# Optimization experiments

Measured on AMD Instinct MI355X. Metric: run time of the kernel, lower is better.

## Reference

```python
import jax, jax.numpy as jnp
import numpy as np
import math

L, D, H = 4, 256, 8
HD = D // H
B, SQ, SK = 2, 1024, 1024
FF = 3 * D
EPS = 1e-5


def setup_inputs() -> dict:
    key = jax.random.key(0)
    ks = jax.random.split(key, 16)
    s = 0.02
    w = lambda k, shape: jax.random.normal(k, shape, jnp.float32) * s
    return {
        "pose": jax.random.normal(ks[0], (B, SQ, D), jnp.float32),
        "vel": jax.random.normal(ks[1], (B, SK, D), jnp.float32),
        "img": jax.random.normal(ks[2], (B, SK, D), jnp.float32),
        "Wq": w(ks[3], (L, D, D)), "bq": jnp.zeros((L, D), jnp.float32),
        "Wk": w(ks[4], (L, D, D)), "bk": jnp.zeros((L, D), jnp.float32),
        "Wv": w(ks[5], (L, D, D)), "bv": jnp.zeros((L, D), jnp.float32),
        "Wo": w(ks[6], (L, D, D)), "bo": jnp.zeros((L, D), jnp.float32),
        "an_g": jnp.ones((L, D), jnp.float32), "an_b": jnp.zeros((L, D), jnp.float32),
        "W1": w(ks[7], (L, D, FF)), "b1": jnp.zeros((L, FF), jnp.float32),
        "W2": w(ks[8], (L, FF, D)), "b2": jnp.zeros((L, D), jnp.float32),
        "fn_g": jnp.ones((L, D), jnp.float32), "fn_b": jnp.zeros((L, D), jnp.float32),
        "n_g": jnp.ones((L, D), jnp.float32), "n_b": jnp.zeros((L, D), jnp.float32),
    }


def entmax15(x):
    # exact alpha=1.5 entmax along the last axis (Peters & Martins 2019)
    x = x * 0.5
    x = x - jnp.max(x, axis=-1, keepdims=True)
    z = -jnp.sort(-x, axis=-1)  # descending
    k = jnp.arange(1, z.shape[-1] + 1, dtype=x.dtype)
    mean = jnp.cumsum(z, axis=-1) / k
    mean_sq = jnp.cumsum(z * z, axis=-1) / k
    ss = k * (mean_sq - mean * mean)
    delta = jnp.clip((1.0 - ss) / k, 0.0)
    tau = mean - jnp.sqrt(delta)
    support = jnp.sum(tau <= z, axis=-1, keepdims=True)  # support size >= 1
    tau_star = jnp.take_along_axis(tau, support - 1, axis=-1)
    p = jnp.clip(x - tau_star, 0.0)
    return p * p


def layer_norm(x, g, b):
    m = jnp.mean(x, axis=-1, keepdims=True)
    v = jnp.mean((x - m) ** 2, axis=-1, keepdims=True)
    return (x - m) * jax.lax.rsqrt(v + EPS) * g + b


def mish(x):
    return x * jnp.tanh(jax.nn.softplus(x))


def reference(pose, vel, img, Wq, bq, Wk, bk, Wv, bv, Wo, bo, an_g, an_b,
              W1, b1, W2, b2, fn_g, fn_b, n_g, n_b):
    def mha(q_in, kv, i):
        bs, sq, _ = q_in.shape
        sk = kv.shape[1]
        q = (q_in @ Wq[i] + bq[i]).reshape(bs, sq, H, HD)
        k = (kv @ Wk[i] + bk[i]).reshape(bs, sk, H, HD)
        v = (kv @ Wv[i] + bv[i]).reshape(bs, sk, H, HD)
        scores = jnp.einsum('bqhd,bkhd->bhqk', q, k) / math.sqrt(HD)
        attn = entmax15(scores)
        out = jnp.einsum('bhqk,bkhd->bqhd', attn, v).reshape(bs, sq, D)
        return out @ Wo[i] + bo[i]

    def cross_layer(x1, x2, i):
        y = layer_norm(mha(x1, x2, i), an_g[i], an_b[i])
        x1 = x1 + y
        y = layer_norm(x1, fn_g[i], fn_b[i])
        h = mish(y @ W1[i] + b1[i]) @ W2[i] + b2[i]
        return x1 + h

    def stack(x, kv):
        for i in range(L):  # small fixed layer loop (shared weights across both paths)
            mem = x
            x = cross_layer(x, kv, i)
            x = layer_norm(x, n_g[i], n_b[i])
            x = x + mem
        return x

    img_out = stack(pose, img)
    pose_out = stack(pose, vel)
    return (pose_out, img_out)
```

## Files before the change

kernel.cpp:

```cpp
#include <hip/hip_runtime.h>
#include <math.h>

#define NL   4
#define DIM  256
#define NH   8
#define HDIM 32
#define SQL  1024
#define SKL  1024
#define FFD  768
#define CB   4
#define ROWS (CB * SQL)

typedef __attribute__((ext_vector_type(8))) short bf16x8;
typedef __attribute__((ext_vector_type(4))) short bf16x4;
typedef __attribute__((ext_vector_type(4))) float f32x4;
typedef __attribute__((ext_vector_type(2))) float f32x2;


__device__ __forceinline__ short f2bf(float f) {
    union { float f; unsigned u; } v; v.f = f;
    unsigned u = v.u + 0x7fffu + ((v.u >> 16) & 1u);
    return (short)(u >> 16);
}

__device__ __forceinline__ float fast_mish(float x) {
    float u = __expf(fminf(x, 20.0f));
    float a = __builtin_fmaf(u, u, 2.0f * u);
    return x * a * __builtin_amdgcn_rcpf(a + 2.0f);
}

__device__ __forceinline__ f32x2 lo2(f32x4 v) { return __builtin_shufflevector(v, v, 0, 1); }
__device__ __forceinline__ f32x2 hi2(f32x4 v) { return __builtin_shufflevector(v, v, 2, 3); }


__global__ __launch_bounds__(256) void init_kernel(
        const float* __restrict__ pose, const float* __restrict__ vel,
        const float* __restrict__ img, float* __restrict__ X,
        short* __restrict__ Xb, short* __restrict__ KVb) {
    int idx = blockIdx.x * 256 + threadIdx.x;
    if (idx >= CB * SQL * DIM) return;
    int c = idx / (SQL * DIM);
    int rem = idx - c * (SQL * DIM);
    int b = c & 1;
    float pv = pose[b * SQL * DIM + rem];
    X[idx]  = pv;
    Xb[idx] = f2bf(pv);
    const float* kv = (c < 2) ? vel : img;
    KVb[idx] = f2bf(kv[b * SQL * DIM + rem]);
}


__global__ __launch_bounds__(256) void transpose_all(
        const float* __restrict__ Wq, const float* __restrict__ Wk,
        const float* __restrict__ Wv, const float* __restrict__ Wo,
        const float* __restrict__ W1, const float* __restrict__ W2,
        short* __restrict__ Wqt, short* __restrict__ Wkt,
        short* __restrict__ Wvt, short* __restrict__ Wot,
        short* __restrict__ W1t, short* __restrict__ W2t) {
    __shared__ float tile[64][65];
    int z = blockIdx.x;
    const float* src; short* dst; int K, N, tx, ty;
    if (z < 256) {
        int m = z >> 6, lyr = (z >> 4) & 3, r = z & 15;
        src = ((m == 0) ? Wq : (m == 1) ? Wk : (m == 2) ? Wv : Wo) + (size_t)lyr * DIM * DIM;
        dst = ((m == 0) ? Wqt : (m == 1) ? Wkt : (m == 2) ? Wvt : Wot) + (size_t)lyr * DIM * DIM;
        K = DIM; N = DIM; tx = r & 3; ty = r >> 2;
    } else if (z < 448) {
        int idx = z - 256, lyr = idx / 48, r = idx % 48;
        src = W1 + (size_t)lyr * DIM * FFD; dst = W1t + (size_t)lyr * DIM * FFD;
        K = DIM; N = FFD; tx = r % 12; ty = r / 12;
    } else {
        int idx = z - 448, lyr = idx / 48, r = idx % 48;
        src = W2 + (size_t)lyr * FFD * DIM; dst = W2t + (size_t)lyr * FFD * DIM;
        K = FFD; N = DIM; tx = r % 4; ty = r / 4;
    }
    int t = threadIdx.x;
    int n0 = tx * 64, k0 = ty * 64;
#pragma unroll
    for (int i = 0; i < 16; i++) {
        int idx = t + i * 256;
        int r = idx >> 6, c = idx & 63;
        tile[r][c] = src[(size_t)(k0 + r) * N + n0 + c];
    }
    __syncthreads();
#pragma unroll
    for (int i = 0; i < 16; i++) {
        int idx = t + i * 256;
        int r = idx >> 6, c = idx & 63;
        dst[(size_t)(n0 + r) * K + k0 + c] = f2bf(tile[c][r]);
    }
}


__global__ __launch_bounds__(256) void qkv_gemm(
        const short* __restrict__ Xb, const short* __restrict__ KVb,
        const short* __restrict__ Wqt, const short* __restrict__ Wkt,
        const short* __restrict__ Wvt,
        const float* __restrict__ bq, const float* __restrict__ bk,
        const float* __restrict__ bv,
        short* __restrict__ Qb, short* __restrict__ Kb, short* __restrict__ Vt,
        float qscale) {
    int z = blockIdx.z;
    const short* A    = (z == 0) ? Xb : KVb;
    const short* Wt   = (z == 0) ? Wqt : (z == 1) ? Wkt : Wvt;
    const float* bias = (z == 0) ? bq : (z == 1) ? bk : bv;
    float scale = (z == 0) ? qscale : 1.0f;

    int t = threadIdx.x, l = t & 63, w = t >> 6;
    int lq = l & 15, lg = l >> 4;
    int bm = blockIdx.y * 64, bn = blockIdx.x * 64;

    const short* ap = A + (size_t)(bm + w * 16 + lq) * DIM + lg * 8;
    const short* wp = Wt + (size_t)(bn + lq) * DIM + lg * 8;

    f32x4 acc[4];
#pragma unroll
    for (int nt = 0; nt < 4; nt++) acc[nt] = (f32x4){0.f, 0.f, 0.f, 0.f};
#pragma unroll
    for (int k0 = 0; k0 < DIM; k0 += 32) {
        bf16x8 af = *(const bf16x8*)(ap + k0);
#pragma unroll
        for (int nt = 0; nt < 4; nt++) {
            bf16x8 bfr = *(const bf16x8*)(wp + (size_t)nt * 16 * DIM + k0);
            acc[nt] = __builtin_amdgcn_mfma_f32_16x16x32_bf16(af, bfr, acc[nt], 0, 0, 0);
        }
    }

    int ms = bm + w * 16 + lg * 4;
#pragma unroll
    for (int nt = 0; nt < 4; nt++) {
        int col = bn + nt * 16 + lq;
        float bv_ = bias[col];
        float v[4];
#pragma unroll
        for (int j = 0; j < 4; j++) v[j] = acc[nt][j] + bv_;
        if (z < 2) {
            short* out = (z == 0) ? Qb : Kb;
#pragma unroll
            for (int j = 0; j < 4; j++) out[(size_t)(ms + j) * DIM + col] = f2bf(v[j] * scale);
        } else {
            int cc = ms >> 10, kl = ms & 1023;
            bf16x4 pk;
#pragma unroll
            for (int j = 0; j < 4; j++) pk[j] = f2bf(v[j]);
            *(bf16x4*)(Vt + ((size_t)(cc * DIM + col)) * SKL + kl) = pk;
        }
    }
}


__global__ __launch_bounds__(512) void fused_tail(
        const short* __restrict__ T1b, const short* __restrict__ Wot,
        const float* __restrict__ bo, const float* __restrict__ Xres,
        const float* __restrict__ ag, const float* __restrict__ ab,
        const float* __restrict__ fg, const float* __restrict__ fb,
        const short* __restrict__ W1t, const float* __restrict__ b1,
        const short* __restrict__ W2t, const float* __restrict__ b2,
        const float* __restrict__ g_, const float* __restrict__ b_,
        float* __restrict__ outf, short* __restrict__ outb) {
    __shared__ float gbuf[16][264];
    __shared__ __align__(16) short y_lds[16][280];
    __shared__ __align__(16) short g1[16][792];
    float (*xbuf)[264] = (float(*)[264])g1;

    int t = threadIdx.x, l = t & 63, w = t >> 6;
    int lq = l & 15, lg = l >> 4;
    int bm = blockIdx.x * 16;

    {
        const short* ap = T1b + (size_t)(bm + lq) * DIM + lg * 8;
        const short* wp = Wot + (size_t)(w * 32 + lq) * DIM + lg * 8;
        f32x4 acc[2];
        acc[0] = (f32x4){0.f, 0.f, 0.f, 0.f};
        acc[1] = (f32x4){0.f, 0.f, 0.f, 0.f};
#pragma unroll
        for (int k0 = 0; k0 < DIM; k0 += 32) {
            bf16x8 af = *(const bf16x8*)(ap + k0);
#pragma unroll
            for (int nt = 0; nt < 2; nt++) {
                bf16x8 bfr = *(const bf16x8*)(wp + (size_t)nt * 16 * DIM + k0);
                acc[nt] = __builtin_amdgcn_mfma_f32_16x16x32_bf16(af, bfr, acc[nt], 0, 0, 0);
            }
        }
#pragma unroll
        for (int nt = 0; nt < 2; nt++) {
            int col = w * 32 + nt * 16 + lq;
            float bv_ = bo[col];
#pragma unroll
            for (int j = 0; j < 4; j++) gbuf[lg * 4 + j][col] = acc[nt][j] + bv_;
        }
    }
    __syncthreads();

    {
        int g = t >> 5, u = t & 31;
        int row = bm + g;
        float s = 0.f, s2 = 0.f;
#pragma unroll
        for (int i = 0; i < 8; i++) {
            float v = gbuf[g][u + 32 * i];
            s += v; s2 += v * v;
        }
#pragma unroll
        for (int off = 1; off < 32; off <<= 1) { s += __shfl_xor(s, off); s2 += __shfl_xor(s2, off); }
        float m = s * (1.f / DIM);
        float rstd = rsqrtf(s2 * (1.f / DIM) - m * m + 1e-5f);

        float x1v[8];
        float sb = 0.f, sb2 = 0.f;
#pragma unroll
        for (int i = 0; i < 8; i++) {
            int col = u + 32 * i;
            float x1 = Xres[(size_t)row * DIM + col] + (gbuf[g][col] - m) * rstd * ag[col] + ab[col];
            x1v[i] = x1; sb += x1; sb2 += x1 * x1;
        }
#pragma unroll
        for (int off = 1; off < 32; off <<= 1) { sb += __shfl_xor(sb, off); sb2 += __shfl_xor(sb2, off); }
        float m2 = sb * (1.f / DIM);
        float rstd2 = rsqrtf(sb2 * (1.f / DIM) - m2 * m2 + 1e-5f);
#pragma unroll
        for (int i = 0; i < 8; i++) {
            int col = u + 32 * i;
            gbuf[g][col]  = x1v[i];
            y_lds[g][col] = f2bf((x1v[i] - m2) * rstd2 * fg[col] + fb[col]);
        }
    }
    __syncthreads();

    {
        const short* wp = W1t + (size_t)(w * 96 + lq) * DIM + lg * 8;
        f32x4 acc[6];
#pragma unroll
        for (int nt = 0; nt < 6; nt++) acc[nt] = (f32x4){0.f, 0.f, 0.f, 0.f};
#pragma unroll
        for (int k0 = 0; k0 < DIM; k0 += 32) {
            bf16x8 af = *(const bf16x8*)(&y_lds[lq][k0 + lg * 8]);
#pragma unroll
            for (int nt = 0; nt < 6; nt++) {
                bf16x8 bfr = *(const bf16x8*)(wp + (size_t)nt * 16 * DIM + k0);
                acc[nt] = __builtin_amdgcn_mfma_f32_16x16x32_bf16(af, bfr, acc[nt], 0, 0, 0);
            }
        }
#pragma unroll
        for (int nt = 0; nt < 6; nt++) {
            int col = w * 96 + nt * 16 + lq;
            float bv_ = b1[col];
#pragma unroll
            for (int j = 0; j < 4; j++)
                g1[lg * 4 + j][col] = f2bf(fast_mish(acc[nt][j] + bv_));
        }
    }
    __syncthreads();

    f32x4 acc2[2];
    acc2[0] = (f32x4){0.f, 0.f, 0.f, 0.f};
    acc2[1] = (f32x4){0.f, 0.f, 0.f, 0.f};
    {
        const short* wp2 = W2t + (size_t)(w * 32 + lq) * FFD + lg * 8;
#pragma unroll 6
        for (int ks = 0; ks < 24; ks++) {
            bf16x8 af = *(const bf16x8*)(&g1[lq][ks * 32 + lg * 8]);
#pragma unroll
            for (int nt = 0; nt < 2; nt++) {
                bf16x8 bfr = *(const bf16x8*)(wp2 + (size_t)nt * 16 * FFD + ks * 32);
                acc2[nt] = __builtin_amdgcn_mfma_f32_16x16x32_bf16(af, bfr, acc2[nt], 0, 0, 0);
            }
        }
    }
    __syncthreads();
#pragma unroll
    for (int nt = 0; nt < 2; nt++) {
        int col = w * 32 + nt * 16 + lq;
        float bv_ = b2[col];
#pragma unroll
        for (int j = 0; j < 4; j++)
            xbuf[lg * 4 + j][col] = acc2[nt][j] + bv_ + gbuf[lg * 4 + j][col];
    }
    __syncthreads();

    {
        int g = t >> 5, u = t & 31;
        int row = bm + g;
        float s = 0.f, s2 = 0.f;
#pragma unroll
        for (int i = 0; i < 8; i++) {
            float v = xbuf[g][u + 32 * i];
            s += v; s2 += v * v;
        }
#pragma unroll
        for (int off = 1; off < 32; off <<= 1) { s += __shfl_xor(s, off); s2 += __shfl_xor(s2, off); }
        float m = s * (1.f / DIM);
        float rstd = rsqrtf(s2 * (1.f / DIM) - m * m + 1e-5f);
#pragma unroll
        for (int i = 0; i < 8; i++) {
            int col = u + 32 * i;
            float o = Xres[(size_t)row * DIM + col] + (xbuf[g][col] - m) * rstd * g_[col] + b_[col];
            outf[(size_t)row * DIM + col] = o;
            if (outb) outb[(size_t)row * DIM + col] = f2bf(o);
        }
    }
}


__global__ __launch_bounds__(512, 6) void attn_mfma(
        const short* __restrict__ Q, const short* __restrict__ K,
        const short* __restrict__ Vt, short* __restrict__ O) {
    int id = blockIdx.x;
    int xcd = id & 7, rest = id >> 3;
    int hc = xcd * 4 + (rest >> 6);
    int c = hc & 3, h = hc >> 2;
    int qbase = (rest & 63) * 16;
    int t = threadIdx.x, l = t & 63, w = t >> 6;
    int lq = l & 15, lg = l >> 4;

    __shared__ __align__(16) short p_lds[8][1024];
    __shared__ float obuf[8][512];
    __shared__ __align__(16) float sred[2][3][16][8];

    bf16x8 qfrag = *(const bf16x8*)(Q + ((size_t)(c * SQL + qbase + lq)) * DIM + h * HDIM + lg * 8);

    const int kw = w * 128;
    f32x4 acc[8];
#pragma unroll
    for (int kt = 0; kt < 8; kt++) {
        bf16x8 kf = *(const bf16x8*)(K + ((size_t)(c * SKL + kw + kt * 16 + lq)) * DIM + h * HDIM + lg * 8);
        f32x4 z = {0.f, 0.f, 0.f, 0.f};
        acc[kt] = __builtin_amdgcn_mfma_f32_16x16x32_bf16(kf, qfrag, z, 0, 0, 0);
    }

    const f32x2 z2  = {0.f, 0.f};
    const f32x2 big = {1e30f, 1e30f};
    const f32x2 one = {1.f, 1.f};

    f32x2 mm = lo2(acc[0]);
#pragma unroll
    for (int kt = 0; kt < 8; kt++) {
        mm = __builtin_elementwise_max(mm, lo2(acc[kt]));
        mm = __builtin_elementwise_max(mm, hi2(acc[kt]));
    }
    float m = fmaxf(mm.x, mm.y);
    m = fmaxf(m, __shfl_xor(m, 16));
    m = fmaxf(m, __shfl_xor(m, 32));
    if (l < 16) sred[1][0][l][w] = m;
    __syncthreads();
    {
        f32x4 a = *(const f32x4*)sred[1][0][lq];
        f32x4 b = *(const f32x4*)(sred[1][0][lq] + 4);
        f32x4 mx = __builtin_elementwise_max(a, b);
        m = fmaxf(fmaxf(mx[0], mx[1]), fmaxf(mx[2], mx[3]));
    }

    float tau = m - 1.0f;
    int r = 0;
    for (;;) {
        f32x2 vt = {tau, tau};
        f32x2 S1 = z2, S2 = z2, NN = z2;
#pragma unroll
        for (int kt = 0; kt < 8; kt++) {
            f32x2 y0 = __builtin_elementwise_max(lo2(acc[kt]) - vt, z2);
            f32x2 y1 = __builtin_elementwise_max(hi2(acc[kt]) - vt, z2);
            S1 += y0; S1 += y1;
            S2 += y0 * y0; S2 += y1 * y1;
            NN += __builtin_elementwise_min(y0 * big, one);
            NN += __builtin_elementwise_min(y1 * big, one);
        }
        float sy = S1.x + S1.y, sy2 = S2.x + S2.y, nn = NN.x + NN.y;
        sy  += __shfl_xor(sy, 16);  sy  += __shfl_xor(sy, 32);
        sy2 += __shfl_xor(sy2, 16); sy2 += __shfl_xor(sy2, 32);
        nn  += __shfl_xor(nn, 16);  nn  += __shfl_xor(nn, 32);
        int b = r & 1;
        if (l < 16) { sred[b][0][l][w] = nn; sred[b][1][l][w] = sy; sred[b][2][l][w] = sy2; }
        __syncthreads();
        {
            f32x4 n0 = *(const f32x4*)sred[b][0][lq];
            f32x4 n1 = *(const f32x4*)(sred[b][0][lq] + 4);
            f32x4 s0 = *(const f32x4*)sred[b][1][lq];
            f32x4 s1 = *(const f32x4*)(sred[b][1][lq] + 4);
            f32x4 q0 = *(const f32x4*)sred[b][2][lq];
            f32x4 q1 = *(const f32x4*)(sred[b][2][lq] + 4);
            f32x4 ns = n0 + n1, ss = s0 + s1, qs = q0 + q1;
            nn  = ns[0] + ns[1] + ns[2] + ns[3];
            sy  = ss[0] + ss[1] + ss[2] + ss[3];
            sy2 = qs[0] + qs[1] + qs[2] + qs[3];
        }
        float disc = fmaxf(sy * sy - nn * (sy2 - 1.0f), 0.f);
        float delta = (sy - sqrtf(disc)) / nn;
        tau = fminf(tau + delta, m - 0.03125f);
        r++;
        if (r >= 6 || __all(delta < 1e-6f)) break;
    }

    f32x4 o0 = {0.f, 0.f, 0.f, 0.f}, o1 = {0.f, 0.f, 0.f, 0.f};
    const short* vbase0 = Vt + ((size_t)(c * DIM + h * HDIM + lq)) * SKL;
    const short* vbase1 = vbase0 + (size_t)16 * SKL;
    {
        f32x2 vt = {tau, tau};
        int swz = (lq & 7) << 4;
#pragma unroll
        for (int c2 = 0; c2 < 2; c2++) {
#pragma unroll
            for (int k4 = 0; k4 < 4; k4++) {
                int kt = c2 * 4 + k4;
                f32x2 y0 = __builtin_elementwise_max(lo2(acc[kt]) - vt, z2);
                f32x2 y1 = __builtin_elementwise_max(hi2(acc[kt]) - vt, z2);
                f32x2 p0 = y0 * y0, p1 = y1 * y1;
                unsigned u01, u23;
                asm("v_cvt_pk_bf16_f32 %0, %1, %2" : "=v"(u01) : "v"(p0.x), "v"(p0.y));
                asm("v_cvt_pk_bf16_f32 %0, %1, %2" : "=v"(u23) : "v"(p1.x), "v"(p1.y));
                int byte = lq * 128 + ((k4 * 32 + lg * 8) ^ swz);
                *(uint2*)((char*)p_lds[w] + byte) = make_uint2(u01, u23);
            }
#pragma unroll
            for (int k2 = 0; k2 < 2; k2++) {
                int byte = lq * 128 + ((k2 * 64 + lg * 16) ^ swz);
                bf16x8 pa = *(const bf16x8*)((const char*)p_lds[w] + byte);
                int k0 = kw + c2 * 64 + k2 * 32 + lg * 8;
                bf16x8 vb0 = *(const bf16x8*)(vbase0 + k0);
                bf16x8 vb1 = *(const bf16x8*)(vbase1 + k0);
                o0 = __builtin_amdgcn_mfma_f32_16x16x32_bf16(pa, vb0, o0, 0, 0, 0);
                o1 = __builtin_amdgcn_mfma_f32_16x16x32_bf16(pa, vb1, o1, 0, 0, 0);
            }
        }
    }

#pragma unroll
    for (int j = 0; j < 4; j++) {
        obuf[w][(lg * 4 + j) * 32 + lq]      = o0[j];
        obuf[w][(lg * 4 + j) * 32 + 16 + lq] = o1[j];
    }
    __syncthreads();
    if (t < 256) {
        int e0 = t * 2;
        int q = e0 >> 5, d = e0 & 31;
        f32x2 s = *(const f32x2*)&obuf[0][e0];
#pragma unroll
        for (int ww = 1; ww < 8; ww++) s += *(const f32x2*)&obuf[ww][e0];
        unsigned uo;
        asm("v_cvt_pk_bf16_f32 %0, %1, %2" : "=v"(uo) : "v"(s.x), "v"(s.y));
        *(unsigned*)(O + ((size_t)(c * SQL + qbase + q)) * DIM + h * HDIM + d) = uo;
    }
}


extern "C" void kernel_launch(void* const* d_in, const int* in_sizes, int n_in,
                              void* d_out, int out_size, void* d_ws, size_t ws_size,
                              hipStream_t stream) {
    const float* pose = (const float*)d_in[0];
    const float* vel  = (const float*)d_in[1];
    const float* img  = (const float*)d_in[2];
    const float* Wq   = (const float*)d_in[3];
    const float* bq   = (const float*)d_in[4];
    const float* Wk   = (const float*)d_in[5];
    const float* bk   = (const float*)d_in[6];
    const float* Wv   = (const float*)d_in[7];
    const float* bv   = (const float*)d_in[8];
    const float* Wo   = (const float*)d_in[9];
    const float* bo   = (const float*)d_in[10];
    const float* an_g = (const float*)d_in[11];
    const float* an_b = (const float*)d_in[12];
    const float* W1   = (const float*)d_in[13];
    const float* b1   = (const float*)d_in[14];
    const float* W2   = (const float*)d_in[15];
    const float* b2   = (const float*)d_in[16];
    const float* fn_g = (const float*)d_in[17];
    const float* fn_b = (const float*)d_in[18];
    const float* n_g  = (const float*)d_in[19];
    const float* n_b  = (const float*)d_in[20];

    const size_t SZ = (size_t)ROWS * DIM;
    float* X    = (float*)d_ws;
    short* Xb   = (short*)(X + SZ);
    short* KVb  = Xb + SZ;
    short* T1b  = KVb + SZ;
    short* Qb   = T1b + SZ;
    short* Kb   = Qb + SZ;
    short* Vt   = Kb + SZ;
    short* Wqt  = Vt + SZ;
    short* Wkt  = Wqt + (size_t)NL * DIM * DIM;
    short* Wvt  = Wkt + (size_t)NL * DIM * DIM;
    short* Wot  = Wvt + (size_t)NL * DIM * DIM;
    short* W1t  = Wot + (size_t)NL * DIM * DIM;
    short* W2t  = W1t + (size_t)NL * DIM * FFD;

    {
        int total = CB * SQL * DIM;
        init_kernel<<<(total + 255) / 256, 256, 0, stream>>>(pose, vel, img, X, Xb, KVb);
    }
    transpose_all<<<640, 256, 0, stream>>>(Wq, Wk, Wv, Wo, W1, W2,
                                           Wqt, Wkt, Wvt, Wot, W1t, W2t);

    const float qscale = 0.08838834764831845f;

    for (int i = 0; i < NL; i++) {
        const short* Wqt_i = Wqt + (size_t)i * DIM * DIM;
        const short* Wkt_i = Wkt + (size_t)i * DIM * DIM;
        const short* Wvt_i = Wvt + (size_t)i * DIM * DIM;
        const short* Wot_i = Wot + (size_t)i * DIM * DIM;
        const short* W1t_i = W1t + (size_t)i * DIM * FFD;
        const short* W2t_i = W2t + (size_t)i * DIM * FFD;

        qkv_gemm<<<dim3(DIM / 64, ROWS / 64, 3), 256, 0, stream>>>(
            Xb, KVb, Wqt_i, Wkt_i, Wvt_i,
            bq + i * DIM, bk + i * DIM, bv + i * DIM, Qb, Kb, Vt, qscale);

        attn_mfma<<<2048, 512, 0, stream>>>(Qb, Kb, Vt, T1b);

        float* outp  = (i == NL - 1) ? (float*)d_out : X;
        short* outbp = (i == NL - 1) ? nullptr : Xb;
        fused_tail<<<ROWS / 16, 512, 0, stream>>>(
            T1b, Wot_i, bo + i * DIM, X,
            an_g + i * DIM, an_b + i * DIM, fn_g + i * DIM, fn_b + i * DIM,
            W1t_i, b1 + i * FFD, W2t_i, b2 + i * DIM,
            n_g + i * DIM, n_b + i * DIM, outp, outbp);
    }

    (void)in_sizes; (void)n_in; (void)out_size; (void)ws_size;
}
```

Baseline: 408.6 us.

## Precompute all-layer K/V projections once and fuse Q projection into attention

K and V depend only on the fixed key/value inputs, so all four layers' K/V projections are now computed up front in one batched kernel launch instead of once per layer. The Q projection is fused into the attention kernel: two waves compute the 16x32 Q tile with MFMA into LDS. This removes one launch per layer and the Q round-trip through global memory. The LDS layout is also reworked, with the reduction buffer transposed, P stored as one 16x128 tile per wave, and obuf aliased onto p_lds, at the cost of an extra barrier, more workspace, and redundant Q computation across blocks that share query rows.

```diff
diff --git a/kernel.cpp b/kernel.cpp
--- a/kernel.cpp
+++ b/kernel.cpp
@@ -92,25 +92,20 @@
 }
 
 
-__global__ __launch_bounds__(256) void qkv_gemm(
-        const short* __restrict__ Xb, const short* __restrict__ KVb,
-        const short* __restrict__ Wqt, const short* __restrict__ Wkt,
-        const short* __restrict__ Wvt,
-        const float* __restrict__ bq, const float* __restrict__ bk,
-        const float* __restrict__ bv,
-        short* __restrict__ Qb, short* __restrict__ Kb, short* __restrict__ Vt,
-        float qscale) {
-    int z = blockIdx.z;
-    const short* A    = (z == 0) ? Xb : KVb;
-    const short* Wt   = (z == 0) ? Wqt : (z == 1) ? Wkt : Wvt;
-    const float* bias = (z == 0) ? bq : (z == 1) ? bk : bv;
-    float scale = (z == 0) ? qscale : 1.0f;
+__global__ __launch_bounds__(256) void kv_gemm(
+        const short* __restrict__ KVb, const short* __restrict__ Wkt,
+        const short* __restrict__ Wvt, const float* __restrict__ bk,
+        const float* __restrict__ bv, short* __restrict__ Kb4,
+        short* __restrict__ Vt4) {
+    int z = blockIdx.z, lyr = z >> 1, kv = z & 1;
+    const short* Wt   = (kv ? Wvt : Wkt) + (size_t)lyr * DIM * DIM;
+    const float* bias = (kv ? bv : bk) + (size_t)lyr * DIM;
 
     int t = threadIdx.x, l = t & 63, w = t >> 6;
     int lq = l & 15, lg = l >> 4;
     int bm = blockIdx.y * 64, bn = blockIdx.x * 64;
 
-    const short* ap = A + (size_t)(bm + w * 16 + lq) * DIM + lg * 8;
+    const short* ap = KVb + (size_t)(bm + w * 16 + lq) * DIM + lg * 8;
     const short* wp = Wt + (size_t)(bn + lq) * DIM + lg * 8;
 
     f32x4 acc[4];
@@ -131,19 +126,17 @@
     for (int nt = 0; nt < 4; nt++) {
         int col = bn + nt * 16 + lq;
         float bv_ = bias[col];
-        float v[4];
-#pragma unroll
-        for (int j = 0; j < 4; j++) v[j] = acc[nt][j] + bv_;
-        if (z < 2) {
-            short* out = (z == 0) ? Qb : Kb;
-#pragma unroll
-            for (int j = 0; j < 4; j++) out[(size_t)(ms + j) * DIM + col] = f2bf(v[j] * scale);
+        if (kv == 0) {
+            short* out = Kb4 + (size_t)lyr * ROWS * DIM;
+#pragma unroll
+            for (int j = 0; j < 4; j++)
+                out[(size_t)(ms + j) * DIM + col] = f2bf(acc[nt][j] + bv_);
         } else {
             int cc = ms >> 10, kl = ms & 1023;
             bf16x4 pk;
 #pragma unroll
-            for (int j = 0; j < 4; j++) pk[j] = f2bf(v[j]);
-            *(bf16x4*)(Vt + ((size_t)(cc * DIM + col)) * SKL + kl) = pk;
+            for (int j = 0; j < 4; j++) pk[j] = f2bf(acc[nt][j] + bv_);
+            *(bf16x4*)(Vt4 + (size_t)lyr * ROWS * DIM + ((size_t)(cc * DIM + col)) * SKL + kl) = pk;
         }
     }
 }
@@ -303,8 +296,9 @@
 
 
 __global__ __launch_bounds__(512, 6) void attn_mfma(
-        const short* __restrict__ Q, const short* __restrict__ K,
-        const short* __restrict__ Vt, short* __restrict__ O) {
+        const short* __restrict__ Xb, const short* __restrict__ Wqt,
+        const float* __restrict__ bq, const short* __restrict__ K,
+        const short* __restrict__ Vt, short* __restrict__ O, float qscale) {
     int id = blockIdx.x;
     int xcd = id & 7, rest = id >> 3;
     int hc = xcd * 4 + (rest >> 6);
@@ -313,11 +307,28 @@
     int t = threadIdx.x, l = t & 63, w = t >> 6;
     int lq = l & 15, lg = l >> 4;
 
-    __shared__ __align__(16) short p_lds[8][1024];
-    __shared__ float obuf[8][512];
-    __shared__ __align__(16) float sred[2][3][16][8];
-
-    bf16x8 qfrag = *(const bf16x8*)(Q + ((size_t)(c * SQL + qbase + lq)) * DIM + h * HDIM + lg * 8);
+    __shared__ __align__(16) short p_lds[8][16 * 128];
+    __shared__ __align__(16) short q_lds[16][40];
+    __shared__ float sred[2][3][8][16];
+    float* obuf = (float*)p_lds;
+
+    if (w < 2) {
+        const short* ap = Xb + (size_t)(c * SQL + qbase + lq) * DIM + lg * 8;
+        const short* wp = Wqt + (size_t)(h * HDIM + w * 16 + lq) * DIM + lg * 8;
+        f32x4 qa = {0.f, 0.f, 0.f, 0.f};
+#pragma unroll
+        for (int k0 = 0; k0 < DIM; k0 += 32) {
+            bf16x8 af = *(const bf16x8*)(ap + k0);
+            bf16x8 bfr = *(const bf16x8*)(wp + k0);
+            qa = __builtin_amdgcn_mfma_f32_16x16x32_bf16(af, bfr, qa, 0, 0, 0);
+        }
+        float bb = bq[h * HDIM + w * 16 + lq];
+#pragma unroll
+        for (int j = 0; j < 4; j++)
+            q_lds[lg * 4 + j][w * 16 + lq] = f2bf((qa[j] + bb) * qscale);
+    }
+    __syncthreads();
+    bf16x8 qfrag = *(const bf16x8*)&q_lds[lq][lg * 8];
 
     const int kw = w * 128;
     f32x4 acc[8];
@@ -341,14 +352,11 @@
     float m = fmaxf(mm.x, mm.y);
     m = fmaxf(m, __shfl_xor(m, 16));
     m = fmaxf(m, __shfl_xor(m, 32));
-    if (l < 16) sred[1][0][l][w] = m;
-    __syncthreads();
-    {
-        f32x4 a = *(const f32x4*)sred[1][0][lq];
-        f32x4 b = *(const f32x4*)(sred[1][0][lq] + 4);
-        f32x4 mx = __builtin_elementwise_max(a, b);
-        m = fmaxf(fmaxf(mx[0], mx[1]), fmaxf(mx[2], mx[3]));
-    }
+    if (l < 16) sred[1][0][w][l] = m;
+    __syncthreads();
+    m = sred[1][0][0][lq];
+#pragma unroll
+    for (int ww = 1; ww < 8; ww++) m = fmaxf(m, sred[1][0][ww][lq]);
 
     float tau = m - 1.0f;
     int r = 0;
@@ -369,19 +377,14 @@
         sy2 += __shfl_xor(sy2, 16); sy2 += __shfl_xor(sy2, 32);
         nn  += __shfl_xor(nn, 16);  nn  += __shfl_xor(nn, 32);
         int b = r & 1;
-        if (l < 16) { sred[b][0][l][w] = nn; sred[b][1][l][w] = sy; sred[b][2][l][w] = sy2; }
+        if (l < 16) { sred[b][0][w][l] = nn; sred[b][1][w][l] = sy; sred[b][2][w][l] = sy2; }
         __syncthreads();
-        {
-            f32x4 n0 = *(const f32x4*)sred[b][0][lq];
-            f32x4 n1 = *(const f32x4*)(sred[b][0][lq] + 4);
-            f32x4 s0 = *(const f32x4*)sred[b][1][lq];
-            f32x4 s1 = *(const f32x4*)(sred[b][1][lq] + 4);
-            f32x4 q0 = *(const f32x4*)sred[b][2][lq];
-            f32x4 q1 = *(const f32x4*)(sred[b][2][lq] + 4);
-            f32x4 ns = n0 + n1, ss = s0 + s1, qs = q0 + q1;
-            nn  = ns[0] + ns[1] + ns[2] + ns[3];
-            sy  = ss[0] + ss[1] + ss[2] + ss[3];
-            sy2 = qs[0] + qs[1] + qs[2] + qs[3];
+        nn = sred[b][0][0][lq]; sy = sred[b][1][0][lq]; sy2 = sred[b][2][0][lq];
+#pragma unroll
+        for (int ww = 1; ww < 8; ww++) {
+            nn  += sred[b][0][ww][lq];
+            sy  += sred[b][1][ww][lq];
+            sy2 += sred[b][2][ww][lq];
         }
         float disc = fmaxf(sy * sy - nn * (sy2 - 1.0f), 0.f);
         float delta = (sy - sqrtf(disc)) / nn;
@@ -395,46 +398,43 @@
     const short* vbase1 = vbase0 + (size_t)16 * SKL;
     {
         f32x2 vt = {tau, tau};
-        int swz = (lq & 7) << 4;
-#pragma unroll
-        for (int c2 = 0; c2 < 2; c2++) {
-#pragma unroll
-            for (int k4 = 0; k4 < 4; k4++) {
-                int kt = c2 * 4 + k4;
-                f32x2 y0 = __builtin_elementwise_max(lo2(acc[kt]) - vt, z2);
-                f32x2 y1 = __builtin_elementwise_max(hi2(acc[kt]) - vt, z2);
-                f32x2 p0 = y0 * y0, p1 = y1 * y1;
-                unsigned u01, u23;
-                asm("v_cvt_pk_bf16_f32 %0, %1, %2" : "=v"(u01) : "v"(p0.x), "v"(p0.y));
-                asm("v_cvt_pk_bf16_f32 %0, %1, %2" : "=v"(u23) : "v"(p1.x), "v"(p1.y));
-                int byte = lq * 128 + ((k4 * 32 + lg * 8) ^ swz);
-                *(uint2*)((char*)p_lds[w] + byte) = make_uint2(u01, u23);
-            }
-#pragma unroll
-            for (int k2 = 0; k2 < 2; k2++) {
-                int byte = lq * 128 + ((k2 * 64 + lg * 16) ^ swz);
-                bf16x8 pa = *(const bf16x8*)((const char*)p_lds[w] + byte);
-                int k0 = kw + c2 * 64 + k2 * 32 + lg * 8;
-                bf16x8 vb0 = *(const bf16x8*)(vbase0 + k0);
-                bf16x8 vb1 = *(const bf16x8*)(vbase1 + k0);
-                o0 = __builtin_amdgcn_mfma_f32_16x16x32_bf16(pa, vb0, o0, 0, 0, 0);
-                o1 = __builtin_amdgcn_mfma_f32_16x16x32_bf16(pa, vb1, o1, 0, 0, 0);
-            }
-        }
-    }
+        int swz = lq << 4;
+#pragma unroll
+        for (int kt = 0; kt < 8; kt++) {
+            f32x2 y0 = __builtin_elementwise_max(lo2(acc[kt]) - vt, z2);
+            f32x2 y1 = __builtin_elementwise_max(hi2(acc[kt]) - vt, z2);
+            f32x2 p0 = y0 * y0, p1 = y1 * y1;
+            unsigned u01, u23;
+            asm("v_cvt_pk_bf16_f32 %0, %1, %2" : "=v"(u01) : "v"(p0.x), "v"(p0.y));
+            asm("v_cvt_pk_bf16_f32 %0, %1, %2" : "=v"(u23) : "v"(p1.x), "v"(p1.y));
+            int byte = lq * 256 + ((kt * 32 + lg * 8) ^ swz);
+            *(uint2*)((char*)p_lds[w] + byte) = make_uint2(u01, u23);
+        }
+#pragma unroll
+        for (int k2 = 0; k2 < 4; k2++) {
+            int byte = lq * 256 + ((k2 * 64 + lg * 16) ^ swz);
+            bf16x8 pa = *(const bf16x8*)((const char*)p_lds[w] + byte);
+            int k0 = kw + k2 * 32 + lg * 8;
+            bf16x8 vb0 = *(const bf16x8*)(vbase0 + k0);
+            bf16x8 vb1 = *(const bf16x8*)(vbase1 + k0);
+            o0 = __builtin_amdgcn_mfma_f32_16x16x32_bf16(pa, vb0, o0, 0, 0, 0);
+            o1 = __builtin_amdgcn_mfma_f32_16x16x32_bf16(pa, vb1, o1, 0, 0, 0);
+        }
+    }
+    __syncthreads();
 
 #pragma unroll
     for (int j = 0; j < 4; j++) {
-        obuf[w][(lg * 4 + j) * 32 + lq]      = o0[j];
-        obuf[w][(lg * 4 + j) * 32 + 16 + lq] = o1[j];
+        obuf[w * 512 + (lg * 4 + j) * 32 + lq]      = o0[j];
+        obuf[w * 512 + (lg * 4 + j) * 32 + 16 + lq] = o1[j];
     }
     __syncthreads();
     if (t < 256) {
         int e0 = t * 2;
         int q = e0 >> 5, d = e0 & 31;
-        f32x2 s = *(const f32x2*)&obuf[0][e0];
-#pragma unroll
-        for (int ww = 1; ww < 8; ww++) s += *(const f32x2*)&obuf[ww][e0];
+        f32x2 s = *(const f32x2*)&obuf[e0];
+#pragma unroll
+        for (int ww = 1; ww < 8; ww++) s += *(const f32x2*)&obuf[ww * 512 + e0];
         unsigned uo;
         asm("v_cvt_pk_bf16_f32 %0, %1, %2" : "=v"(uo) : "v"(s.x), "v"(s.y));
         *(unsigned*)(O + ((size_t)(c * SQL + qbase + q)) * DIM + h * HDIM + d) = uo;
@@ -472,10 +472,9 @@
     short* Xb   = (short*)(X + SZ);
     short* KVb  = Xb + SZ;
     short* T1b  = KVb + SZ;
-    short* Qb   = T1b + SZ;
-    short* Kb   = Qb + SZ;
-    short* Vt   = Kb + SZ;
-    short* Wqt  = Vt + SZ;
+    short* Kb4  = T1b + SZ;
+    short* Vt4  = Kb4 + (size_t)NL * SZ;
+    short* Wqt  = Vt4 + (size_t)NL * SZ;
     short* Wkt  = Wqt + (size_t)NL * DIM * DIM;
     short* Wvt  = Wkt + (size_t)NL * DIM * DIM;
     short* Wot  = Wvt + (size_t)NL * DIM * DIM;
@@ -488,22 +487,20 @@
     }
     transpose_all<<<640, 256, 0, stream>>>(Wq, Wk, Wv, Wo, W1, W2,
                                            Wqt, Wkt, Wvt, Wot, W1t, W2t);
+    kv_gemm<<<dim3(DIM / 64, ROWS / 64, 2 * NL), 256, 0, stream>>>(
+        KVb, Wkt, Wvt, bk, bv, Kb4, Vt4);
 
     const float qscale = 0.08838834764831845f;
 
     for (int i = 0; i < NL; i++) {
         const short* Wqt_i = Wqt + (size_t)i * DIM * DIM;
-        const short* Wkt_i = Wkt + (size_t)i * DIM * DIM;
-        const short* Wvt_i = Wvt + (size_t)i * DIM * DIM;
         const short* Wot_i = Wot + (size_t)i * DIM * DIM;
         const short* W1t_i = W1t + (size_t)i * DIM * FFD;
         const short* W2t_i = W2t + (size_t)i * DIM * FFD;
 
-        qkv_gemm<<<dim3(DIM / 64, ROWS / 64, 3), 256, 0, stream>>>(
-            Xb, KVb, Wqt_i, Wkt_i, Wvt_i,
-            bq + i * DIM, bk + i * DIM, bv + i * DIM, Qb, Kb, Vt, qscale);
-
-        attn_mfma<<<2048, 512, 0, stream>>>(Qb, Kb, Vt, T1b);
+        attn_mfma<<<2048, 512, 0, stream>>>(
+            Xb, Wqt_i, bq + i * DIM, Kb4 + (size_t)i * SZ, Vt4 + (size_t)i * SZ,
+            T1b, qscale);
 
         float* outp  = (i == NL - 1) ? (float*)d_out : X;
         short* outbp = (i == NL - 1) ? nullptr : Xb;
```

After: 394.7 us. -3.4%, faster.
